# Performance work log

Hardware: AMD Instinct MI355X
Metric: run time of the kernel (lower is better)

Reference implementation:

```python
import jax, jax.numpy as jnp
import numpy as np

N_NODES = 50000
N_EDGES = 1600000  # avg degree 32
IN_FEAT = 128
OUT_FEAT = 128


def setup_inputs() -> dict:
    key = jax.random.key(0)
    k1, k2, k3, k4 = jax.random.split(key, 4)
    features = jax.random.normal(k1, (N_NODES, IN_FEAT), dtype=jnp.float32)
    # GlorotUniform-scale weight
    limit = np.sqrt(6.0 / (IN_FEAT + OUT_FEAT)).astype(np.float32)
    weight = jax.random.uniform(k2, (IN_FEAT, OUT_FEAT), dtype=jnp.float32,
                                minval=-limit, maxval=limit)
    edge_src = jax.random.randint(k3, (N_EDGES,), 0, N_NODES, dtype=jnp.int32)
    edge_dst = jax.random.randint(k4, (N_EDGES,), 0, N_NODES, dtype=jnp.int32)
    return {"features": features, "weight": weight,
            "edge_src": edge_src, "edge_dst": edge_dst}


def reference(features, weight, edge_src, edge_dst):
    # self representation: [N, out_feat]
    nodes_rep = features @ weight
    # gather neighbor features at edge sources: [E, in_feat]
    neighbor_repr = features[edge_src]
    # unsorted_segment_mean over destination indices
    seg_sum = jax.ops.segment_sum(neighbor_repr, edge_dst, num_segments=N_NODES)
    counts = jax.ops.segment_sum(jnp.ones((edge_dst.shape[0], 1), features.dtype),
                                 edge_dst, num_segments=N_NODES)
    agg = seg_sum / jnp.maximum(counts, 1.0)
    # transform aggregated messages with the shared weight: [N, out_feat]
    agg_rep = agg @ weight
    # combination_type == 'concat' -> [N, 2*out_feat], then activation
    h = jnp.concatenate([nodes_rep, agg_rep], axis=-1)
    return jax.nn.relu(h)
```

## Files before the change

kernel.cpp:

```cpp
#include <hip/hip_runtime.h>
#include <hip/hip_fp16.h>

#define N_NODES 50000
#define N_EDGES 1600000
#define FEAT 128
#define CAP 80
#define NRANGE 4
#define NODE_RANGE 12500


__global__ __launch_bounds__(256) void fill_kernel(const int* __restrict__ src,
                                                   const int* __restrict__ dst,
                                                   int* __restrict__ cursor,
                                                   unsigned short* __restrict__ csr, int n) {
    const int r = blockIdx.x & (NRANGE - 1);
    const int lo = r * NODE_RANGE;
    const int nchunk = gridDim.x / NRANGE;
    const int j = blockIdx.x / NRANGE;
    const int stride = nchunk * 256;
    for (int i = j * 256 + threadIdx.x; i < n; i += stride) {
        int d = __builtin_nontemporal_load(&dst[i]);
        if ((unsigned)(d - lo) < (unsigned)NODE_RANGE) {
            int s = __builtin_nontemporal_load(&src[i]);
            int p = atomicAdd(&cursor[d], 1);
            if (p < CAP) csr[d * CAP + p] = (unsigned short)s;
        }
    }
}


__global__ __launch_bounds__(256, 2) void gemmP_kernel(const float* __restrict__ feat,
                                                       const float* __restrict__ W,
                                                       __half* __restrict__ Ph,
                                                       float* __restrict__ out) {
    __shared__ float Wl[FEAT * FEAT];
    __shared__ float At[FEAT * 32];
    const int tid = threadIdx.x;

    for (int idx = tid; idx < FEAT * FEAT / 4; idx += 256)
        ((float4*)Wl)[idx] = ((const float4*)W)[idx];

    const int row0 = blockIdx.x * 32;
    {
        const int row = tid >> 3;
        const int kb = (tid & 7) * 16;
        const int grow = row0 + row;
        float4 a0 = {0,0,0,0}, a1 = {0,0,0,0}, a2 = {0,0,0,0}, a3 = {0,0,0,0};
        if (grow < N_NODES) {
            const float* src = feat + (size_t)grow * FEAT + kb;
            a0 = ((const float4*)src)[0];
            a1 = ((const float4*)src)[1];
            a2 = ((const float4*)src)[2];
            a3 = ((const float4*)src)[3];
        }
        float* dst = &At[row];
        dst[(kb + 0) * 32] = a0.x;  dst[(kb + 1) * 32] = a0.y;
        dst[(kb + 2) * 32] = a0.z;  dst[(kb + 3) * 32] = a0.w;
        dst[(kb + 4) * 32] = a1.x;  dst[(kb + 5) * 32] = a1.y;
        dst[(kb + 6) * 32] = a1.z;  dst[(kb + 7) * 32] = a1.w;
        dst[(kb + 8) * 32] = a2.x;  dst[(kb + 9) * 32] = a2.y;
        dst[(kb + 10) * 32] = a2.z; dst[(kb + 11) * 32] = a2.w;
        dst[(kb + 12) * 32] = a3.x; dst[(kb + 13) * 32] = a3.y;
        dst[(kb + 14) * 32] = a3.z; dst[(kb + 15) * 32] = a3.w;
    }
    __syncthreads();

    const int lane = tid & 63;
    const int wv = tid >> 6;
    const int colg = lane & 15;
    const int rowg = lane >> 4;
    const int rbase = (wv >> 1) * 16;
    const int col = (wv & 1) * 64 + colg * 4;

    float4 acc0 = {0,0,0,0}, acc1 = {0,0,0,0}, acc2 = {0,0,0,0}, acc3 = {0,0,0,0};
    const float* at = &At[rbase + rowg * 4];
    const float* wp = &Wl[col];

#pragma unroll 4
    for (int k = 0; k < FEAT; ++k) {
        float4 a = *(const float4*)(at + k * 32);
        float4 w = *(const float4*)(wp + k * 128);
        acc0.x += a.x * w.x; acc0.y += a.x * w.y; acc0.z += a.x * w.z; acc0.w += a.x * w.w;
        acc1.x += a.y * w.x; acc1.y += a.y * w.y; acc1.z += a.y * w.z; acc1.w += a.y * w.w;
        acc2.x += a.z * w.x; acc2.y += a.z * w.y; acc2.z += a.z * w.z; acc2.w += a.z * w.w;
        acc3.x += a.w * w.x; acc3.y += a.w * w.y; acc3.z += a.w * w.z; acc3.w += a.w * w.w;
    }

    float4 r[4] = {acc0, acc1, acc2, acc3};
#pragma unroll
    for (int i = 0; i < 4; ++i) {
        int row = row0 + rbase + rowg * 4 + i;
        if (row < N_NODES) {
            float4 v = r[i];
            union { __half2 h2[2]; uint2 u; } pk;
            pk.h2[0] = __floats2half2_rn(v.x, v.y);
            pk.h2[1] = __floats2half2_rn(v.z, v.w);
            *(uint2*)&Ph[(size_t)row * FEAT + col] = pk.u;
            v.x = fmaxf(v.x, 0.f); v.y = fmaxf(v.y, 0.f);
            v.z = fmaxf(v.z, 0.f); v.w = fmaxf(v.w, 0.f);
            *(float4*)&out[(size_t)row * 256 + col] = v;
        }
    }
}


__global__ __launch_bounds__(256) void gather_kernel(const __half* __restrict__ Ph,
                                                     const int* __restrict__ cursor,
                                                     const unsigned short* __restrict__ csr,
                                                     float* __restrict__ out) {
    const int lane = threadIdx.x & 63;
    const int wid = (blockIdx.x * blockDim.x + threadIdx.x) >> 6;
    const int nw = (gridDim.x * blockDim.x) >> 6;
    for (int node = wid; node < N_NODES; node += nw) {
        const int deg = cursor[node];
        const unsigned short* row = &csr[node * CAP];
        float x = 0.f, y = 0.f;
        int j = 0;
        for (; j + 4 <= deg; j += 4) {
            int s0 = row[j], s1 = row[j + 1], s2 = row[j + 2], s3 = row[j + 3];
            float2 v0 = __half22float2(*(const __half2*)&Ph[(size_t)s0 * FEAT + 2 * lane]);
            float2 v1 = __half22float2(*(const __half2*)&Ph[(size_t)s1 * FEAT + 2 * lane]);
            float2 v2 = __half22float2(*(const __half2*)&Ph[(size_t)s2 * FEAT + 2 * lane]);
            float2 v3 = __half22float2(*(const __half2*)&Ph[(size_t)s3 * FEAT + 2 * lane]);
            x += v0.x + v1.x + v2.x + v3.x;
            y += v0.y + v1.y + v2.y + v3.y;
        }
        for (; j < deg; ++j) {
            int s = row[j];
            float2 v = __half22float2(*(const __half2*)&Ph[(size_t)s * FEAT + 2 * lane]);
            x += v.x;
            y += v.y;
        }
        float scale = 1.0f / (float)(deg > 1 ? deg : 1);
        float2 o = make_float2(fmaxf(x * scale, 0.f), fmaxf(y * scale, 0.f));
        *(float2*)&out[(size_t)node * 256 + FEAT + 2 * lane] = o;
    }
}


extern "C" void kernel_launch(void* const* d_in, const int* in_sizes, int n_in,
                              void* d_out, int out_size, void* d_ws, size_t ws_size,
                              hipStream_t stream) {
    const float* feat = (const float*)d_in[0];
    const float* W = (const float*)d_in[1];
    const int* esrc = (const int*)d_in[2];
    const int* edst = (const int*)d_in[3];
    float* out = (float*)d_out;

    char* ws = (char*)d_ws;
    int* cursor = (int*)(ws + 0);
    unsigned short* csr = (unsigned short*)(ws + 200704);
    __half* Ph  = (__half*)(ws + 200704 + 8000000);

    hipMemsetAsync(ws, 0, 200000, stream);

    fill_kernel<<<2048, 256, 0, stream>>>(esrc, edst, cursor, csr, N_EDGES);
    gemmP_kernel<<<(N_NODES + 31) / 32, 256, 0, stream>>>(feat, W, Ph, out);
    gather_kernel<<<12500, 256, 0, stream>>>(Ph, cursor, csr, out);
}
```

Baseline: 256.7 us.

## Replace global-atomic CSR fill with two-pass bucketed partition in shared memory

Replaces the single fill kernel, which did a global atomic per edge into per-node cursors, with a two-phase partition. Phase A buckets edges by dst>>8 using shared-memory histograms, one global atomic per bucket per block, and packs (bucket, local dst, src) into 32-bit entries. Phase B builds each 256-node CSR slab in LDS and writes it out coalesced together with clamped degrees. This removes heavy global atomic contention and scattered 2-byte writes, at the cost of an extra pass over a 6.8MB intermediate buffer and a bucket capacity limit (BCAP) that could drop edges on skewed inputs.

```diff
diff --git a/kernel.cpp b/kernel.cpp
--- a/kernel.cpp
+++ b/kernel.cpp
@@ -5,27 +5,81 @@
 #define N_EDGES 1600000
 #define FEAT 128
 #define CAP 80
-#define NRANGE 4
-#define NODE_RANGE 12500
-
-
-__global__ __launch_bounds__(256) void fill_kernel(const int* __restrict__ src,
-                                                   const int* __restrict__ dst,
-                                                   int* __restrict__ cursor,
-                                                   unsigned short* __restrict__ csr, int n) {
-    const int r = blockIdx.x & (NRANGE - 1);
-    const int lo = r * NODE_RANGE;
-    const int nchunk = gridDim.x / NRANGE;
-    const int j = blockIdx.x / NRANGE;
-    const int stride = nchunk * 256;
-    for (int i = j * 256 + threadIdx.x; i < n; i += stride) {
-        int d = __builtin_nontemporal_load(&dst[i]);
-        if ((unsigned)(d - lo) < (unsigned)NODE_RANGE) {
+#define NB 196
+#define BCAP 8704
+#define CHUNK 6250
+
+
+__global__ __launch_bounds__(256) void partA_kernel(const int* __restrict__ src,
+                                                    const int* __restrict__ dst,
+                                                    int* __restrict__ bcur,
+                                                    unsigned int* __restrict__ sorted, int n) {
+    __shared__ unsigned int stage[CHUNK + 6];
+    __shared__ int hist[NB], base[NB], cur[NB];
+    const int t = threadIdx.x;
+    for (int b = t; b < NB; b += 256) hist[b] = 0;
+    __syncthreads();
+
+    const int start = blockIdx.x * CHUNK;
+    const int m = min(CHUNK, n - start);
+#pragma unroll
+    for (int k = 0; k < 25; ++k) {
+        int idx = k * 256 + t;
+        if (idx < m) {
+            int i = start + idx;
+            int d = __builtin_nontemporal_load(&dst[i]);
             int s = __builtin_nontemporal_load(&src[i]);
-            int p = atomicAdd(&cursor[d], 1);
-            if (p < CAP) csr[d * CAP + p] = (unsigned short)s;
-        }
-    }
+            int b = d >> 8;
+            atomicAdd(&hist[b], 1);
+            stage[idx] = ((unsigned)b << 24) | ((unsigned)(d & 255) << 16) | (unsigned)s;
+        }
+    }
+    __syncthreads();
+    for (int b = t; b < NB; b += 256) {
+        base[b] = atomicAdd(&bcur[b], hist[b]);
+        cur[b] = 0;
+    }
+    __syncthreads();
+#pragma unroll
+    for (int k = 0; k < 25; ++k) {
+        int idx = k * 256 + t;
+        if (idx < m) {
+            unsigned e = stage[idx];
+            int b = e >> 24;
+            int p = base[b] + atomicAdd(&cur[b], 1);
+            if (p < BCAP) sorted[(size_t)b * BCAP + p] = e;
+        }
+    }
+}
+
+
+__global__ __launch_bounds__(256) void partB_kernel(const unsigned int* __restrict__ sorted,
+                                                    const int* __restrict__ bcur,
+                                                    unsigned short* __restrict__ csr,
+                                                    int* __restrict__ deg) {
+    __shared__ unsigned short csr_s[256 * CAP];
+    __shared__ int cur[256];
+    const int b = blockIdx.x;
+    const int t = threadIdx.x;
+    cur[t] = 0;
+    __syncthreads();
+
+    const int nb = min(bcur[b], BCAP);
+    const unsigned int* ebase = &sorted[(size_t)b * BCAP];
+    for (int i = t; i < nb; i += 256) {
+        unsigned e = ebase[i];
+        int dl = (e >> 16) & 255;
+        int p = atomicAdd(&cur[dl], 1);
+        if (p < CAP) csr_s[dl * CAP + p] = (unsigned short)(e & 0xFFFFu);
+    }
+    __syncthreads();
+
+    const int node0 = b << 8;
+    int node = node0 + t;
+    if (node < N_NODES) deg[node] = min(cur[t], CAP);
+    unsigned int* g = (unsigned int*)&csr[(size_t)node0 * CAP];
+    const unsigned int* ls = (const unsigned int*)csr_s;
+    for (int i = t; i < 256 * CAP / 2; i += 256) g[i] = ls[i];
 }
 
 
@@ -47,21 +101,21 @@
         const int grow = row0 + row;
         float4 a0 = {0,0,0,0}, a1 = {0,0,0,0}, a2 = {0,0,0,0}, a3 = {0,0,0,0};
         if (grow < N_NODES) {
-            const float* src = feat + (size_t)grow * FEAT + kb;
-            a0 = ((const float4*)src)[0];
-            a1 = ((const float4*)src)[1];
-            a2 = ((const float4*)src)[2];
-            a3 = ((const float4*)src)[3];
-        }
-        float* dst = &At[row];
-        dst[(kb + 0) * 32] = a0.x;  dst[(kb + 1) * 32] = a0.y;
-        dst[(kb + 2) * 32] = a0.z;  dst[(kb + 3) * 32] = a0.w;
-        dst[(kb + 4) * 32] = a1.x;  dst[(kb + 5) * 32] = a1.y;
-        dst[(kb + 6) * 32] = a1.z;  dst[(kb + 7) * 32] = a1.w;
-        dst[(kb + 8) * 32] = a2.x;  dst[(kb + 9) * 32] = a2.y;
-        dst[(kb + 10) * 32] = a2.z; dst[(kb + 11) * 32] = a2.w;
-        dst[(kb + 12) * 32] = a3.x; dst[(kb + 13) * 32] = a3.y;
-        dst[(kb + 14) * 32] = a3.z; dst[(kb + 15) * 32] = a3.w;
+            const float* srcp = feat + (size_t)grow * FEAT + kb;
+            a0 = ((const float4*)srcp)[0];
+            a1 = ((const float4*)srcp)[1];
+            a2 = ((const float4*)srcp)[2];
+            a3 = ((const float4*)srcp)[3];
+        }
+        float* dstp = &At[row];
+        dstp[(kb + 0) * 32] = a0.x;  dstp[(kb + 1) * 32] = a0.y;
+        dstp[(kb + 2) * 32] = a0.z;  dstp[(kb + 3) * 32] = a0.w;
+        dstp[(kb + 4) * 32] = a1.x;  dstp[(kb + 5) * 32] = a1.y;
+        dstp[(kb + 6) * 32] = a1.z;  dstp[(kb + 7) * 32] = a1.w;
+        dstp[(kb + 8) * 32] = a2.x;  dstp[(kb + 9) * 32] = a2.y;
+        dstp[(kb + 10) * 32] = a2.z; dstp[(kb + 11) * 32] = a2.w;
+        dstp[(kb + 12) * 32] = a3.x; dstp[(kb + 13) * 32] = a3.y;
+        dstp[(kb + 14) * 32] = a3.z; dstp[(kb + 15) * 32] = a3.w;
     }
     __syncthreads();
 
@@ -105,15 +159,15 @@
 
 
 __global__ __launch_bounds__(256) void gather_kernel(const __half* __restrict__ Ph,
-                                                     const int* __restrict__ cursor,
+                                                     const int* __restrict__ deg_arr,
                                                      const unsigned short* __restrict__ csr,
                                                      float* __restrict__ out) {
     const int lane = threadIdx.x & 63;
     const int wid = (blockIdx.x * blockDim.x + threadIdx.x) >> 6;
     const int nw = (gridDim.x * blockDim.x) >> 6;
     for (int node = wid; node < N_NODES; node += nw) {
-        const int deg = cursor[node];
-        const unsigned short* row = &csr[node * CAP];
+        const int deg = deg_arr[node];
+        const unsigned short* row = &csr[(size_t)node * CAP];
         float x = 0.f, y = 0.f;
         int j = 0;
         for (; j + 4 <= deg; j += 4) {
@@ -148,13 +202,16 @@
     float* out = (float*)d_out;
 
     char* ws = (char*)d_ws;
-    int* cursor = (int*)(ws + 0);
-    unsigned short* csr = (unsigned short*)(ws + 200704);
-    __half* Ph  = (__half*)(ws + 200704 + 8000000);
-
-    hipMemsetAsync(ws, 0, 200000, stream);
-
-    fill_kernel<<<2048, 256, 0, stream>>>(esrc, edst, cursor, csr, N_EDGES);
+    int* bcur = (int*)(ws + 0);
+    unsigned int* sorted = (unsigned int*)(ws + 4096);
+    unsigned short* csr = (unsigned short*)(ws + 6828032);
+    int* deg = (int*)(ws + 14856192);
+    __half* Ph = (__half*)(ws + 15060992);
+
+    hipMemsetAsync(ws, 0, 4096, stream);
+
+    partA_kernel<<<256, 256, 0, stream>>>(esrc, edst, bcur, sorted, N_EDGES);
+    partB_kernel<<<NB, 256, 0, stream>>>(sorted, bcur, csr, deg);
     gemmP_kernel<<<(N_NODES + 31) / 32, 256, 0, stream>>>(feat, W, Ph, out);
-    gather_kernel<<<12500, 256, 0, stream>>>(Ph, cursor, csr, out);
-}
+    gather_kernel<<<12500, 256, 0, stream>>>(Ph, deg, csr, out);
+}
```

Measured after the change: 216.7 us. 1.18x faster.
